# Kernel optimization log

Measured on AMD Instinct MI355X. Metric: run time of the kernel, lower is better.

Reference implementation:

```python
import jax, jax.numpy as jnp
import numpy as np

N, E = 25000, 400000
F, D, H, C, L = 64, 128, 4, 128, 3  # in_feat, hidden, heads, per-head dim, layers
SCALE = 1.0 / np.sqrt(C)

_PNAMES = [f"{nm}{l}" for l in range(L) for nm in ("Wq", "bq", "Wk", "bk", "Wv", "bv", "Ws", "bs")]


def setup_inputs() -> dict:
    key = jax.random.key(0)
    ks = jax.random.split(key, 64)
    inp = {
        "x": jax.random.normal(ks[0], (N, F), jnp.float32),
        "edge_index": jax.random.randint(ks[1], (2, E), 0, N, jnp.int32),
    }
    i = 2
    for l in range(L):
        fin = F if l == 0 else D
        s = 1.0 / np.sqrt(fin)
        shapes = {"Wq": (fin, H * C), "bq": (H * C,), "Wk": (fin, H * C), "bk": (H * C,),
                  "Wv": (fin, H * C), "bv": (H * C,), "Ws": (fin, D), "bs": (D,)}
        for nm, shp in shapes.items():
            scale = s if nm.startswith("W") else 0.01
            inp[f"{nm}{l}"] = jax.random.normal(ks[i], shp, jnp.float32) * scale
            i += 1
    inp["Wfc"] = jax.random.normal(ks[i], (D, 1), jnp.float32) * (1.0 / np.sqrt(D))
    inp["bfc"] = jnp.zeros((1,), jnp.float32)
    return inp


def _conv(x, src, dst, Wq, bq, Wk, bk, Wv, bv, Ws, bs):
    """PyG TransformerConv, heads=H, concat=False (head-mean), root_weight=True."""
    n = x.shape[0]
    q = (x @ Wq + bq).reshape(n, H, C)
    k = (x @ Wk + bk).reshape(n, H, C)
    v = (x @ Wv + bv).reshape(n, H, C)
    # per-edge attention logits: query at dst, key at src  -> [E, H]
    alpha = jnp.einsum("ehc,ehc->eh", q[dst], k[src]) * SCALE
    # scatter-softmax over incoming edges of each destination node
    m = jax.ops.segment_max(alpha, dst, num_segments=n)        # [N, H]
    e = jnp.exp(alpha - m[dst])                                 # [E, H]
    denom = jax.ops.segment_sum(e, dst, num_segments=n)        # [N, H]
    a = e / (denom[dst] + 1e-16)                                # [E, H]
    out = jax.ops.segment_sum(a[:, :, None] * v[src], dst, num_segments=n)  # [N, H, C]
    return out.mean(axis=1) + x @ Ws + bs                       # concat=False -> mean heads; + skip


def reference(x, edge_index,
              Wq0, bq0, Wk0, bk0, Wv0, bv0, Ws0, bs0,
              Wq1, bq1, Wk1, bk1, Wv1, bv1, Ws1, bs1,
              Wq2, bq2, Wk2, bk2, Wv2, bv2, Ws2, bs2,
              Wfc, bfc):
    src, dst = edge_index[0], edge_index[1]
    h = jax.nn.relu(_conv(x, src, dst, Wq0, bq0, Wk0, bk0, Wv0, bv0, Ws0, bs0))
    h = jax.nn.relu(_conv(h, src, dst, Wq1, bq1, Wk1, bk1, Wv1, bv1, Ws1, bs1))
    h = jax.nn.relu(_conv(h, src, dst, Wq2, bq2, Wk2, bk2, Wv2, bv2, Ws2, bs2))
    g = h.mean(axis=0, keepdims=True)                           # [1, D]
    return jax.nn.sigmoid(g @ Wfc + bfc)                        # [1, 1]
```

## Files before the change

### kernel.cpp

```cpp
#include <hip/hip_runtime.h>
#include <hip/hip_bf16.h>
#include <math.h>

#define NNODES 25000
#define NEDGES 400000
#define FIN0 64
#define DHID 128
#define NHEAD 4
#define CDIM 128
#define HC (NHEAD * CDIM)
#define NOUT 1664
#define SCALE 0.088388347648318447f

typedef __attribute__((ext_vector_type(8))) short short8;
typedef __attribute__((ext_vector_type(4))) float floatx4;
typedef __attribute__((ext_vector_type(2))) float fx2;

__device__ __forceinline__ short f2bf(float v) {
    unsigned u = __float_as_uint(v);
    u = (u + 0x7fffu + ((u >> 16) & 1u)) >> 16;
    return (short)u;
}
__device__ __forceinline__ float bf2f(short s) {
    return __uint_as_float(((unsigned)(unsigned short)s) << 16);
}


__global__ void cvt_x_kernel(const float* __restrict__ x, short* __restrict__ xb, int total) {
    int i = blockIdx.x * blockDim.x + threadIdx.x;
    if (i < total) xb[i] = f2bf(x[i]);
}

__global__ __launch_bounds__(256) void cvt_w_kernel(
    const float* __restrict__ Wq, const float* __restrict__ Wk,
    const float* __restrict__ Wv, const float* __restrict__ Ws,
    const float* __restrict__ bq, const float* __restrict__ bk,
    const float* __restrict__ bv, const float* __restrict__ bs,
    short* __restrict__ WT, float* __restrict__ bc, int fin)
{
    __shared__ float tile[32][33];
    int c0 = blockIdx.x * 32;
    int k0 = blockIdx.y * 32;
    int tx = threadIdx.x & 31, ty = threadIdx.x >> 5;

    const float* W; int ldw, cb;
    if (c0 < 512)       { W = Wq; ldw = 512; cb = c0; }
    else if (c0 < 1024) { W = Wk; ldw = 512; cb = c0 - 512; }
    else if (c0 < 1536) { W = Wv; ldw = 512; cb = c0 - 1024; }
    else                { W = Ws; ldw = 128; cb = c0 - 1536; }

#pragma unroll
    for (int i = 0; i < 4; ++i) {
        int k = k0 + ty + i * 8;
        tile[ty + i * 8][tx] = W[(size_t)k * ldw + cb + tx];
    }
    __syncthreads();
#pragma unroll
    for (int i = 0; i < 4; ++i) {
        int c = c0 + ty + i * 8;
        WT[(size_t)c * fin + k0 + tx] = f2bf(tile[tx][ty + i * 8]);
    }

    if (blockIdx.y == 0 && ty == 0) {
        int c = c0 + tx;
        float b;
        if (c < 512)       b = bq[c];
        else if (c < 1024) b = bk[c - 512];
        else if (c < 1536) b = bv[c - 1024];
        else               b = bs[c - 1536];
        bc[c] = b;
    }
}


__global__ void count_kernel(const int* __restrict__ dst, int* __restrict__ deg, int e) {
    int i = blockIdx.x * blockDim.x + threadIdx.x;
    if (i < e) atomicAdd(&deg[dst[i]], 1);
}

__global__ void scan_kernel(const int* __restrict__ deg, int* __restrict__ offs,
                            int* __restrict__ cnt, int n, int total) {
    __shared__ int sums[256];
    int t = threadIdx.x;
    int chunk = (n + 255) / 256;
    int b = t * chunk;
    int e = min(b + chunk, n);
    int s = 0;
    for (int i = b; i < e; ++i) s += deg[i];
    sums[t] = s;
    __syncthreads();
    for (int o = 1; o < 256; o <<= 1) {
        int v = (t >= o) ? sums[t - o] : 0;
        __syncthreads();
        sums[t] += v;
        __syncthreads();
    }
    int run = sums[t] - s;
    for (int i = b; i < e; ++i) {
        offs[i] = run;
        run += deg[i];
        cnt[i] = 0;
    }
    if (t == 0) offs[n] = total;
}

__global__ void scatter_kernel(const int* __restrict__ src, const int* __restrict__ dst,
                               const int* __restrict__ offs, int* __restrict__ cnt,
                               int* __restrict__ csr, int e) {
    int i = blockIdx.x * blockDim.x + threadIdx.x;
    if (i < e) {
        int d = dst[i];
        int pos = offs[d] + atomicAdd(&cnt[d], 1);
        csr[pos] = src[i];
    }
}

template<int FIN>
__global__ __launch_bounds__(256) void gemm_qkvs_mfma(
    const short* __restrict__ Xb, int n,
    const short* __restrict__ WT, const float* __restrict__ bc,
    short* __restrict__ Qb, unsigned char* __restrict__ KV,
    short* __restrict__ Sb)
{
    constexpr int PITCH = FIN + 8;
    constexpr int CPR = FIN / 8;
    constexpr int NK = FIN / 32;
    __shared__ short Xs[64][PITCH];

    int t = threadIdx.x;
    int row0 = blockIdx.x * 64;
    int l = t & 63, w = t >> 6;
    int lr = l & 15, lk = (l >> 4) * 8;
    int cl = lr, rb = (l >> 4) * 4;

    for (int i = t; i < 64 * CPR; i += 256) {
        int r = i / CPR, c = (i % CPR) * 8;
        int gr = row0 + r;
        uint4 v = make_uint4(0u, 0u, 0u, 0u);
        if (gr < n) v = *(const uint4*)&Xb[(size_t)gr * FIN + c];
        *(uint4*)&Xs[r][c] = v;
    }
    __syncthreads();

    for (int y = 0; y < 7; ++y) {
        int wcol = y * 256 + w * 64;
        if (wcol >= NOUT) continue;

        float bias[4];
#pragma unroll
        for (int ni = 0; ni < 4; ++ni) bias[ni] = bc[wcol + ni * 16 + cl];

        floatx4 acc[4][4] = {};
#pragma unroll
        for (int ks = 0; ks < NK; ++ks) {
            short8 b[4];
#pragma unroll
            for (int ni = 0; ni < 4; ++ni)
                b[ni] = *(const short8*)&WT[(size_t)(wcol + ni * 16 + lr) * FIN + ks * 32 + lk];
            short8 a[4];
#pragma unroll
            for (int mi = 0; mi < 4; ++mi)
                a[mi] = *(const short8*)&Xs[mi * 16 + lr][ks * 32 + lk];
#pragma unroll
            for (int mi = 0; mi < 4; ++mi)
#pragma unroll
                for (int ni = 0; ni < 4; ++ni)
                    acc[mi][ni] = __builtin_amdgcn_mfma_f32_16x16x32_bf16(
                        a[mi], b[ni], acc[mi][ni], 0, 0, 0);
        }

        int kind = (wcol < 512) ? 0 : (wcol < 1024) ? 1 : (wcol < 1536) ? 2 : 3;
#pragma unroll
        for (int mi = 0; mi < 4; ++mi) {
#pragma unroll
            for (int ni = 0; ni < 4; ++ni) {
                int gc = wcol + ni * 16 + cl;
#pragma unroll
                for (int r = 0; r < 4; ++r) {
                    int gr = row0 + mi * 16 + rb + r;
                    if (gr >= n) continue;
                    float v = acc[mi][ni][r] + bias[ni];
                    if (kind == 0) {
                        Qb[(size_t)gr * 512 + gc] = f2bf(v);
                    } else if (kind == 1) {
                        unsigned enc = (unsigned)__builtin_amdgcn_cvt_pk_fp8_f32(v, v, 0, false);
                        KV[(size_t)gr * 1024 + (gc - 512)] = (unsigned char)enc;
                    } else if (kind == 2) {
                        unsigned enc = (unsigned)__builtin_amdgcn_cvt_pk_fp8_f32(v, v, 0, false);
                        KV[(size_t)gr * 1024 + 512 + (gc - 1024)] = (unsigned char)enc;
                    } else {
                        Sb[(size_t)gr * 128 + (gc - 1536)] = f2bf(v);
                    }
                }
            }
        }
    }
}


__device__ __forceinline__ void unpack8(uint4 r, float* f) {
    f[0] = __uint_as_float(r.x << 16);
    f[1] = __uint_as_float(r.x & 0xffff0000u);
    f[2] = __uint_as_float(r.y << 16);
    f[3] = __uint_as_float(r.y & 0xffff0000u);
    f[4] = __uint_as_float(r.z << 16);
    f[5] = __uint_as_float(r.z & 0xffff0000u);
    f[6] = __uint_as_float(r.w << 16);
    f[7] = __uint_as_float(r.w & 0xffff0000u);
}

__device__ __forceinline__ void decf8(unsigned x, unsigned y, float* f) {
    fx2 a = __builtin_amdgcn_cvt_pk_f32_fp8(x, false);
    fx2 b = __builtin_amdgcn_cvt_pk_f32_fp8(x, true);
    fx2 c = __builtin_amdgcn_cvt_pk_f32_fp8(y, false);
    fx2 d = __builtin_amdgcn_cvt_pk_f32_fp8(y, true);
    f[0] = a[0]; f[1] = a[1]; f[2] = b[0]; f[3] = b[1];
    f[4] = c[0]; f[5] = c[1]; f[6] = d[0]; f[7] = d[1];
}

__device__ __forceinline__ float dotk(const float* q, uint2 kr) {
    float f[8];
    decf8(kr.x, kr.y, f);
    float p = 0.f;
#pragma unroll
    for (int j = 0; j < 8; ++j) p = fmaf(q[j], f[j], p);
    return p;
}

__device__ __forceinline__ void accv(float& d, float* acc, float p, uint2 vr) {
    float vf[8];
    decf8(vr.x, vr.y, vf);
    float w = __expf(p * SCALE);
    d += w;
#pragma unroll
    for (int j = 0; j < 8; ++j) acc[j] = fmaf(w, vf[j], acc[j]);
}

__device__ __forceinline__ float redu16(float p) {
#pragma unroll
    for (int o = 1; o < 16; o <<= 1) p += __shfl_xor(p, o);
    return p;
}

__global__ __launch_bounds__(256) void attn_kernel(
    const short* __restrict__ Qb, const unsigned char* __restrict__ KV,
    const int* __restrict__ offs, const int* __restrict__ csr,
    const short* __restrict__ Sb, short* __restrict__ Xo, int n)
{
    int node = (blockIdx.x * blockDim.x + threadIdx.x) >> 6;
    if (node >= n) return;
    int lane = threadIdx.x & 63;

    float qf[8];
    {
        uint4 qr = *(const uint4*)&Qb[(size_t)node * 512 + lane * 8];
        unpack8(qr, qf);
    }

    int beg = offs[node], end = offs[node + 1];
    float d = 0.f;
    float acc[8] = {};

    int e = beg;
    for (; e + 7 < end; e += 8) {
        uint2 kr[8], vr[8];
#pragma unroll
        for (int j = 0; j < 8; ++j) {
            int s = csr[e + j];
            const unsigned char* b = KV + (size_t)s * 1024 + lane * 8;
            kr[j] = *(const uint2*)b;
            vr[j] = *(const uint2*)(b + 512);
        }
        float p[8];
#pragma unroll
        for (int j = 0; j < 8; ++j) p[j] = dotk(qf, kr[j]);
#pragma unroll
        for (int j = 0; j < 8; ++j) p[j] = redu16(p[j]);
#pragma unroll
        for (int j = 0; j < 8; ++j) accv(d, acc, p[j], vr[j]);
    }
    for (; e + 3 < end; e += 4) {
        uint2 kr[4], vr[4];
#pragma unroll
        for (int j = 0; j < 4; ++j) {
            int s = csr[e + j];
            const unsigned char* b = KV + (size_t)s * 1024 + lane * 8;
            kr[j] = *(const uint2*)b;
            vr[j] = *(const uint2*)(b + 512);
        }
        float p[4];
#pragma unroll
        for (int j = 0; j < 4; ++j) p[j] = dotk(qf, kr[j]);
#pragma unroll
        for (int j = 0; j < 4; ++j) p[j] = redu16(p[j]);
#pragma unroll
        for (int j = 0; j < 4; ++j) accv(d, acc, p[j], vr[j]);
    }
    for (; e < end; ++e) {
        int s = csr[e];
        const unsigned char* b = KV + (size_t)s * 1024 + lane * 8;
        uint2 kr = *(const uint2*)b;
        uint2 vr = *(const uint2*)(b + 512);
        float p = redu16(dotk(qf, kr));
        accv(d, acc, p, vr);
    }

    float inv = (d > 0.f) ? 1.f / d : 0.f;
#pragma unroll
    for (int j = 0; j < 8; ++j) acc[j] *= inv;

#pragma unroll
    for (int j = 0; j < 8; ++j) {
        acc[j] += __shfl_xor(acc[j], 16);
        acc[j] += __shfl_xor(acc[j], 32);
    }

    if (lane < 16) {
        int c0 = lane * 8;
        float sf[8];
        uint4 sr = *(const uint4*)&Sb[(size_t)node * 128 + c0];
        unpack8(sr, sf);
        short8 o;
#pragma unroll
        for (int j = 0; j < 8; ++j)
            o[j] = f2bf(fmaxf(acc[j] * 0.25f + sf[j], 0.f));
        *(short8*)&Xo[(size_t)node * 128 + c0] = o;
    }
}

__global__ void colsum_kernel(const short* __restrict__ X, float* __restrict__ g, int n) {
    int c = threadIdx.x;
    int rpb = (n + gridDim.x - 1) / gridDim.x;
    int r0 = blockIdx.x * rpb;
    int r1 = min(r0 + rpb, n);
    float acc = 0.f;
    for (int r = r0; r < r1; ++r) acc += bf2f(X[r * DHID + c]);
    atomicAdd(&g[c], acc);
}

__global__ void final_kernel(const float* __restrict__ g, const float* __restrict__ Wfc,
                             const float* __restrict__ bfc, float* __restrict__ out, float invn) {
    __shared__ float red[128];
    int t = threadIdx.x;
    red[t] = g[t] * invn * Wfc[t];
    __syncthreads();
    for (int o = 64; o > 0; o >>= 1) {
        if (t < o) red[t] += red[t + o];
        __syncthreads();
    }
    if (t == 0) {
        float z = red[0] + bfc[0];
        out[0] = 1.f / (1.f + expf(-z));
    }
}


extern "C" void kernel_launch(void* const* d_in, const int* in_sizes, int n_in,
                              void* d_out, int out_size, void* d_ws, size_t ws_size,
                              hipStream_t stream) {
    const int N = NNODES, E = NEDGES;
    const float* x = (const float*)d_in[0];
    const int* ei = (const int*)d_in[1];
    const int* src = ei;
    const int* dst = ei + E;
    const float* Wfc = (const float*)d_in[26];
    const float* bfc = (const float*)d_in[27];

    size_t off = 0;
    auto alloc = [&](size_t bytes) -> char* {
        char* p = (char*)d_ws + off;
        off += (bytes + 255) & ~(size_t)255;
        return p;
    };
    int* deg   = (int*)alloc((size_t)N * 4);
    int* cnt   = (int*)alloc((size_t)N * 4);
    int* offs  = (int*)alloc((size_t)(N + 1) * 4);
    int* csr   = (int*)alloc((size_t)E * 4);
    short* Qb  = (short*)alloc((size_t)N * HC * 2);
    unsigned char* KV = (unsigned char*)alloc((size_t)N * 1024);
    short* Sb  = (short*)alloc((size_t)N * DHID * 2);
    short* xb0 = (short*)alloc((size_t)(N + 64) * FIN0 * 2);
    short* xb1 = (short*)alloc((size_t)(N + 64) * DHID * 2);
    short* xb2 = (short*)alloc((size_t)(N + 64) * DHID * 2);
    short* WT  = (short*)alloc((size_t)NOUT * DHID * 2);
    float* bc  = (float*)alloc((size_t)NOUT * 4);
    float* g   = (float*)alloc(128 * 4);

    hipMemsetAsync(deg, 0, (size_t)N * 4, stream);
    hipMemsetAsync(g, 0, 128 * 4, stream);

    count_kernel<<<(E + 255) / 256, 256, 0, stream>>>(dst, deg, E);
    scan_kernel<<<1, 256, 0, stream>>>(deg, offs, cnt, N, E);
    scatter_kernel<<<(E + 255) / 256, 256, 0, stream>>>(src, dst, offs, cnt, csr, E);

    cvt_x_kernel<<<(N * FIN0 + 255) / 256, 256, 0, stream>>>(x, xb0, N * FIN0);

    int attn_blocks = (N + 3) / 4;

    const short* xin = xb0;
    short* xouts[3] = { xb1, xb2, xb1 };
    for (int l = 0; l < 3; ++l) {
        int fin = (l == 0) ? FIN0 : DHID;
        const float* Wq = (const float*)d_in[2 + l * 8 + 0];
        const float* bq = (const float*)d_in[2 + l * 8 + 1];
        const float* Wk = (const float*)d_in[2 + l * 8 + 2];
        const float* bk = (const float*)d_in[2 + l * 8 + 3];
        const float* Wv = (const float*)d_in[2 + l * 8 + 4];
        const float* bv = (const float*)d_in[2 + l * 8 + 5];
        const float* Wss= (const float*)d_in[2 + l * 8 + 6];
        const float* bs = (const float*)d_in[2 + l * 8 + 7];

        dim3 wgrid(NOUT / 32, fin / 32);
        cvt_w_kernel<<<wgrid, 256, 0, stream>>>(
            Wq, Wk, Wv, Wss, bq, bk, bv, bs, WT, bc, fin);

        int gblocks = (N + 63) / 64;
        if (l == 0)
            gemm_qkvs_mfma<64><<<gblocks, 256, 0, stream>>>(xin, N, WT, bc, Qb, KV, Sb);
        else
            gemm_qkvs_mfma<128><<<gblocks, 256, 0, stream>>>(xin, N, WT, bc, Qb, KV, Sb);
        attn_kernel<<<attn_blocks, 256, 0, stream>>>(Qb, KV, offs, csr, Sb, xouts[l], N);
        xin = xouts[l];
    }

    colsum_kernel<<<256, 128, 0, stream>>>(xb1, g, N);
    final_kernel<<<1, 128, 0, stream>>>(g, Wfc, bfc, (float*)d_out, 1.0f / N);
}
```

Baseline: 642.4 us.

## Fuse input fp32->bf16 conversion into GEMM, split output columns across grid, vectorize stores

Removes the separate x-to-bf16 conversion kernel by converting fp32 rows while staging them into shared memory in the first layer's GEMM. The GEMM grid gains a second dimension so each block handles one 256-column slice instead of looping over all seven, which raises parallelism but makes each block reload its X tile. MFMA operands are swapped so each lane holds four consecutive output columns, allowing packed bf16/fp8 conversion and vectorized 8- and 4-byte stores in place of scalar byte/short stores. The scan kernel is widened to 1024 threads.

```diff
diff --git a/kernel.cpp b/kernel.cpp
--- a/kernel.cpp
+++ b/kernel.cpp
@@ -24,12 +24,12 @@
 __device__ __forceinline__ float bf2f(short s) {
     return __uint_as_float(((unsigned)(unsigned short)s) << 16);
 }
-
-
-__global__ void cvt_x_kernel(const float* __restrict__ x, short* __restrict__ xb, int total) {
-    int i = blockIdx.x * blockDim.x + threadIdx.x;
-    if (i < total) xb[i] = f2bf(x[i]);
-}
+__device__ __forceinline__ unsigned cvt_pk_bf16(float lo, float hi) {
+    unsigned r;
+    asm("v_cvt_pk_bf16_f32 %0, %1, %2" : "=v"(r) : "v"(lo), "v"(hi));
+    return r;
+}
+
 
 __global__ __launch_bounds__(256) void cvt_w_kernel(
     const float* __restrict__ Wq, const float* __restrict__ Wk,
@@ -78,18 +78,19 @@
     if (i < e) atomicAdd(&deg[dst[i]], 1);
 }
 
-__global__ void scan_kernel(const int* __restrict__ deg, int* __restrict__ offs,
-                            int* __restrict__ cnt, int n, int total) {
-    __shared__ int sums[256];
+__global__ __launch_bounds__(1024) void scan_kernel(
+    const int* __restrict__ deg, int* __restrict__ offs,
+    int* __restrict__ cnt, int n, int total) {
+    __shared__ int sums[1024];
     int t = threadIdx.x;
-    int chunk = (n + 255) / 256;
+    int chunk = (n + 1023) / 1024;
     int b = t * chunk;
     int e = min(b + chunk, n);
     int s = 0;
     for (int i = b; i < e; ++i) s += deg[i];
     sums[t] = s;
     __syncthreads();
-    for (int o = 1; o < 256; o <<= 1) {
+    for (int o = 1; o < 1024; o <<= 1) {
         int v = (t >= o) ? sums[t - o] : 0;
         __syncthreads();
         sums[t] += v;
@@ -115,9 +116,9 @@
     }
 }
 
-template<int FIN>
+template<int FIN, bool CVT>
 __global__ __launch_bounds__(256) void gemm_qkvs_mfma(
-    const short* __restrict__ Xb, int n,
+    const void* __restrict__ Xsrc, int n,
     const short* __restrict__ WT, const float* __restrict__ bc,
     short* __restrict__ Qb, unsigned char* __restrict__ KV,
     short* __restrict__ Sb)
@@ -130,68 +131,88 @@
     int t = threadIdx.x;
     int row0 = blockIdx.x * 64;
     int l = t & 63, w = t >> 6;
+    int wcol = blockIdx.y * 256 + w * 64;
+    bool active = (wcol < NOUT);
     int lr = l & 15, lk = (l >> 4) * 8;
-    int cl = lr, rb = (l >> 4) * 4;
+    int cg = (l >> 4) * 4;
 
     for (int i = t; i < 64 * CPR; i += 256) {
         int r = i / CPR, c = (i % CPR) * 8;
         int gr = row0 + r;
-        uint4 v = make_uint4(0u, 0u, 0u, 0u);
-        if (gr < n) v = *(const uint4*)&Xb[(size_t)gr * FIN + c];
-        *(uint4*)&Xs[r][c] = v;
+        if (CVT) {
+            const float* xf = (const float*)Xsrc;
+            short8 s = {};
+            if (gr < n) {
+                float4 f0 = *(const float4*)&xf[(size_t)gr * FIN + c];
+                float4 f1 = *(const float4*)&xf[(size_t)gr * FIN + c + 4];
+                s[0] = f2bf(f0.x); s[1] = f2bf(f0.y); s[2] = f2bf(f0.z); s[3] = f2bf(f0.w);
+                s[4] = f2bf(f1.x); s[5] = f2bf(f1.y); s[6] = f2bf(f1.z); s[7] = f2bf(f1.w);
+            }
+            *(short8*)&Xs[r][c] = s;
+        } else {
+            const short* xb = (const short*)Xsrc;
+            uint4 v = make_uint4(0u, 0u, 0u, 0u);
+            if (gr < n) v = *(const uint4*)&xb[(size_t)gr * FIN + c];
+            *(uint4*)&Xs[r][c] = v;
+        }
     }
     __syncthreads();
-
-    for (int y = 0; y < 7; ++y) {
-        int wcol = y * 256 + w * 64;
-        if (wcol >= NOUT) continue;
-
-        float bias[4];
-#pragma unroll
-        for (int ni = 0; ni < 4; ++ni) bias[ni] = bc[wcol + ni * 16 + cl];
-
-        floatx4 acc[4][4] = {};
-#pragma unroll
-        for (int ks = 0; ks < NK; ++ks) {
-            short8 b[4];
+    if (!active) return;
+
+    float4 bias[4];
+#pragma unroll
+    for (int ni = 0; ni < 4; ++ni)
+        bias[ni] = *(const float4*)&bc[wcol + ni * 16 + cg];
+
+    floatx4 acc[4][4] = {};
+#pragma unroll
+    for (int ks = 0; ks < NK; ++ks) {
+        short8 b[4];
+#pragma unroll
+        for (int ni = 0; ni < 4; ++ni)
+            b[ni] = *(const short8*)&WT[(size_t)(wcol + ni * 16 + lr) * FIN + ks * 32 + lk];
+        short8 a[4];
+#pragma unroll
+        for (int mi = 0; mi < 4; ++mi)
+            a[mi] = *(const short8*)&Xs[mi * 16 + lr][ks * 32 + lk];
+#pragma unroll
+        for (int mi = 0; mi < 4; ++mi)
 #pragma unroll
             for (int ni = 0; ni < 4; ++ni)
-                b[ni] = *(const short8*)&WT[(size_t)(wcol + ni * 16 + lr) * FIN + ks * 32 + lk];
-            short8 a[4];
-#pragma unroll
-            for (int mi = 0; mi < 4; ++mi)
-                a[mi] = *(const short8*)&Xs[mi * 16 + lr][ks * 32 + lk];
-#pragma unroll
-            for (int mi = 0; mi < 4; ++mi)
-#pragma unroll
-                for (int ni = 0; ni < 4; ++ni)
-                    acc[mi][ni] = __builtin_amdgcn_mfma_f32_16x16x32_bf16(
-                        a[mi], b[ni], acc[mi][ni], 0, 0, 0);
-        }
-
-        int kind = (wcol < 512) ? 0 : (wcol < 1024) ? 1 : (wcol < 1536) ? 2 : 3;
-#pragma unroll
-        for (int mi = 0; mi < 4; ++mi) {
-#pragma unroll
-            for (int ni = 0; ni < 4; ++ni) {
-                int gc = wcol + ni * 16 + cl;
-#pragma unroll
-                for (int r = 0; r < 4; ++r) {
-                    int gr = row0 + mi * 16 + rb + r;
-                    if (gr >= n) continue;
-                    float v = acc[mi][ni][r] + bias[ni];
-                    if (kind == 0) {
-                        Qb[(size_t)gr * 512 + gc] = f2bf(v);
-                    } else if (kind == 1) {
-                        unsigned enc = (unsigned)__builtin_amdgcn_cvt_pk_fp8_f32(v, v, 0, false);
-                        KV[(size_t)gr * 1024 + (gc - 512)] = (unsigned char)enc;
-                    } else if (kind == 2) {
-                        unsigned enc = (unsigned)__builtin_amdgcn_cvt_pk_fp8_f32(v, v, 0, false);
-                        KV[(size_t)gr * 1024 + 512 + (gc - 1024)] = (unsigned char)enc;
-                    } else {
-                        Sb[(size_t)gr * 128 + (gc - 1536)] = f2bf(v);
-                    }
-                }
+                acc[mi][ni] = __builtin_amdgcn_mfma_f32_16x16x32_bf16(
+                    b[ni], a[mi], acc[mi][ni], 0, 0, 0);
+    }
+
+    int kind = (wcol < 512) ? 0 : (wcol < 1024) ? 1 : (wcol < 1536) ? 2 : 3;
+#pragma unroll
+    for (int mi = 0; mi < 4; ++mi) {
+        int gr = row0 + mi * 16 + lr;
+        if (gr >= n) continue;
+#pragma unroll
+        for (int ni = 0; ni < 4; ++ni) {
+            int gc = wcol + ni * 16 + cg;
+            float v0 = acc[mi][ni][0] + bias[ni].x;
+            float v1 = acc[mi][ni][1] + bias[ni].y;
+            float v2 = acc[mi][ni][2] + bias[ni].z;
+            float v3 = acc[mi][ni][3] + bias[ni].w;
+            if (kind == 0) {
+                uint2 p;
+                p.x = cvt_pk_bf16(v0, v1);
+                p.y = cvt_pk_bf16(v2, v3);
+                *(uint2*)&Qb[(size_t)gr * 512 + gc] = p;
+            } else if (kind == 1) {
+                unsigned r8 = (unsigned)__builtin_amdgcn_cvt_pk_fp8_f32(v0, v1, 0, false);
+                r8 = (unsigned)__builtin_amdgcn_cvt_pk_fp8_f32(v2, v3, r8, true);
+                *(unsigned*)&KV[(size_t)gr * 1024 + (gc - 512)] = r8;
+            } else if (kind == 2) {
+                unsigned r8 = (unsigned)__builtin_amdgcn_cvt_pk_fp8_f32(v0, v1, 0, false);
+                r8 = (unsigned)__builtin_amdgcn_cvt_pk_fp8_f32(v2, v3, r8, true);
+                *(unsigned*)&KV[(size_t)gr * 1024 + 512 + (gc - 1024)] = r8;
+            } else {
+                uint2 p;
+                p.x = cvt_pk_bf16(v0, v1);
+                p.y = cvt_pk_bf16(v2, v3);
+                *(uint2*)&Sb[(size_t)gr * 128 + (gc - 1536)] = p;
             }
         }
     }
@@ -379,7 +400,6 @@
     short* Qb  = (short*)alloc((size_t)N * HC * 2);
     unsigned char* KV = (unsigned char*)alloc((size_t)N * 1024);
     short* Sb  = (short*)alloc((size_t)N * DHID * 2);
-    short* xb0 = (short*)alloc((size_t)(N + 64) * FIN0 * 2);
     short* xb1 = (short*)alloc((size_t)(N + 64) * DHID * 2);
     short* xb2 = (short*)alloc((size_t)(N + 64) * DHID * 2);
     short* WT  = (short*)alloc((size_t)NOUT * DHID * 2);
@@ -390,14 +410,13 @@
     hipMemsetAsync(g, 0, 128 * 4, stream);
 
     count_kernel<<<(E + 255) / 256, 256, 0, stream>>>(dst, deg, E);
-    scan_kernel<<<1, 256, 0, stream>>>(deg, offs, cnt, N, E);
+    scan_kernel<<<1, 1024, 0, stream>>>(deg, offs, cnt, N, E);
     scatter_kernel<<<(E + 255) / 256, 256, 0, stream>>>(src, dst, offs, cnt, csr, E);
 
-    cvt_x_kernel<<<(N * FIN0 + 255) / 256, 256, 0, stream>>>(x, xb0, N * FIN0);
-
     int attn_blocks = (N + 3) / 4;
-
-    const short* xin = xb0;
+    int gx = (N + 63) / 64;
+
+    const void* xin = x;
     short* xouts[3] = { xb1, xb2, xb1 };
     for (int l = 0; l < 3; ++l) {
         int fin = (l == 0) ? FIN0 : DHID;
@@ -414,11 +433,11 @@
         cvt_w_kernel<<<wgrid, 256, 0, stream>>>(
             Wq, Wk, Wv, Wss, bq, bk, bv, bs, WT, bc, fin);
 
-        int gblocks = (N + 63) / 64;
+        dim3 ggrid(gx, 7);
         if (l == 0)
-            gemm_qkvs_mfma<64><<<gblocks, 256, 0, stream>>>(xin, N, WT, bc, Qb, KV, Sb);
+            gemm_qkvs_mfma<64, true><<<ggrid, 256, 0, stream>>>(xin, N, WT, bc, Qb, KV, Sb);
         else
-            gemm_qkvs_mfma<128><<<gblocks, 256, 0, stream>>>(xin, N, WT, bc, Qb, KV, Sb);
+            gemm_qkvs_mfma<128, false><<<ggrid, 256, 0, stream>>>(xin, N, WT, bc, Qb, KV, Sb);
         attn_kernel<<<attn_blocks, 256, 0, stream>>>(Qb, KV, offs, csr, Sb, xouts[l], N);
         xin = xouts[l];
     }
```

Measured after the change: 562.5 us. 12.4% less time.
